# Kernel optimization log

Hardware: AMD Instinct MI355X
Metric: run time of the kernel (lower is better)

Reference implementation:

```python
import jax, jax.numpy as jnp
import numpy as np

N_VERT = 1000          # num_of_vertices; x has 3*N_VERT rows
B = 32                 # batch
IN_DIM = 64
OUT_DIMS = [64, 64, 64]


def setup_inputs() -> dict:
    key = jax.random.key(0)
    ks = jax.random.split(key, 8)
    threeN = 3 * N_VERT
    x = jax.random.normal(ks[0], (threeN, B, IN_DIM), dtype=jnp.float32)
    # dense (normalized-ish) adjacency over the localized spatio-temporal graph
    adj = jax.random.uniform(ks[1], (threeN, threeN), dtype=jnp.float32) / threeN
    inp = {"x": x, "adj": adj}
    in_d = IN_DIM
    for i, out_d in enumerate(OUT_DIMS):
        # torch Linear(in_d, 2*out_d): store as [in_d, 2*out_d] for x @ W + b
        scale = 1.0 / np.sqrt(in_d)
        inp[f"W{i}"] = jax.random.uniform(ks[2 + 2 * i], (in_d, 2 * out_d),
                                          minval=-scale, maxval=scale, dtype=jnp.float32)
        inp[f"b{i}"] = jax.random.uniform(ks[3 + 2 * i], (2 * out_d,),
                                          minval=-scale, maxval=scale, dtype=jnp.float32)
        in_d = out_d
    return inp


def _gcn_glu(adj, x, W, b, out_dim):
    # aggregate: [3N,3N] x [3N,B,C] -> [3N,B,C]
    h = jnp.einsum('nm,mbc->nbc', adj, x)
    lr = h @ W + b                       # [3N,B,2*out]
    lhs, rhs = lr[..., :out_dim], lr[..., out_dim:]
    return lhs * jax.nn.sigmoid(rhs)     # GLU


def reference(x, adj, W0, b0, W1, b1, W2, b2):
    n = x.shape[0] // 3
    Ws = [(W0, b0), (W1, b1), (W2, b2)]
    mids = []
    h = x
    for (W, b), out_d in zip(Ws, OUT_DIMS):
        h = _gcn_glu(adj, h, W, b, out_d)
        mids.append(h[n:2 * n])          # middle time-step slice [N,B,out]
    return jnp.max(jnp.stack(mids, axis=0), axis=0)  # [N,B,out]
```

## Files before the change

### kernel.cpp

```cpp
#include <hip/hip_runtime.h>
#include <stdint.h>
#include <math.h>

#define NV   3000
#define MP   3072
#define NBC  2048
#define NMID 1000

typedef unsigned short u16;
typedef short  s8vec __attribute__((ext_vector_type(8)));
typedef float  f4vec __attribute__((ext_vector_type(4)));


__device__ __forceinline__ u16 f2b(float f) {
  union { float f; unsigned int u; } v; v.f = f;
  unsigned int r = v.u + 0x7FFFu + ((v.u >> 16) & 1u);
  return (u16)(r >> 16);
}
__device__ __forceinline__ float b2f(u16 u) {
  union { unsigned int u; float f; } v; v.u = ((unsigned int)u) << 16;
  return v.f;
}

__device__ __forceinline__ void gload16(const void* g, void* l) {
  __builtin_amdgcn_global_load_lds(
      (const __attribute__((address_space(1))) void*)g,
      (__attribute__((address_space(3))) void*)l, 16, 0, 0);
}

__global__ void k_conv_adj(const float* __restrict__ adj,
                           u16* __restrict__ adjt) {
  __shared__ __align__(16) u16 tb[64][80];
  const int bx = blockIdx.x;
  const int by = blockIdx.y;
  const int t  = threadIdx.x;

  {
    const int rl = t >> 2, quad = t & 3;
    const int r  = by * 64 + rl;
    const bool rok = (r < NV);
#pragma unroll
    for (int i = 0; i < 4; ++i) {
      int c = bx * 64 + quad * 16 + i * 4;
      float4 f = {0.f, 0.f, 0.f, 0.f};
      if (rok && c < NV) f = *(const float4*)(adj + (size_t)r * NV + c);
      ushort4 o;
      o.x = f2b(f.x); o.y = f2b(f.y); o.z = f2b(f.z); o.w = f2b(f.w);
      *(ushort4*)&tb[rl][quad * 16 + i * 4] = o;
    }
  }
  __syncthreads();

  {
#pragma unroll
    for (int h = 0; h < 2; ++h) {
      int chunk = t * 2 + h;
      int sel  = chunk >> 8;
      int g    = (chunk >> 6) & 3;
      int lane = chunk & 63;
      int row  = g * 16 + (lane & 15);
      int col  = sel * 32 + (lane >> 4) * 8;
      s8vec v = *(const s8vec*)&tb[row][col];
      size_t dst = ((size_t)(by * 96 + bx * 2 + sel) * 4 + g) * 512 + lane * 8;
      *(s8vec*)(adjt + dst) = v;
    }
  }
}

__global__ void k_conv_x(const float* __restrict__ x,
                         u16* __restrict__ xt) {
  __shared__ __align__(16) u16 tb[64][72];
  int t  = threadIdx.x;
  int k0 = blockIdx.x * 64;
  int n0 = blockIdx.y * 64;
  int kl = t >> 4, ch = t & 15;
#pragma unroll
  for (int r = 0; r < 4; ++r) {
    int k = k0 + kl + r * 16;
    float4 f = {0.f, 0.f, 0.f, 0.f};
    if (k < NV) f = *(const float4*)(x + (size_t)k * NBC + n0 + ch * 4);
    tb[ch * 4 + 0][kl + r * 16] = f2b(f.x);
    tb[ch * 4 + 1][kl + r * 16] = f2b(f.y);
    tb[ch * 4 + 2][kl + r * 16] = f2b(f.z);
    tb[ch * 4 + 3][kl + r * 16] = f2b(f.w);
  }
  __syncthreads();
  int nl = t >> 4, kc = t & 15;
#pragma unroll
  for (int r = 0; r < 4; ++r) {
    int n = n0 + nl + r * 16;
    int k = k0 + kc * 4;
    ushort4 o;
    o.x = tb[nl + r * 16][kc * 4 + 0];
    o.y = tb[nl + r * 16][kc * 4 + 1];
    o.z = tb[nl + r * 16][kc * 4 + 2];
    o.w = tb[nl + r * 16][kc * 4 + 3];
    int nt = n >> 7, g = (n >> 4) & 7, lr = n & 15;
    int kk = k >> 5, hi = (k >> 3) & 3, j = k & 7;
    size_t dst = ((size_t)(nt * 96 + kk) * 8 + g) * 512 +
                 (size_t)(hi * 16 + lr) * 8 + j;
    *(ushort4*)(xt + dst) = o;
  }
}

__global__ void k_conv_w(const float* __restrict__ W0,
                         const float* __restrict__ W1,
                         const float* __restrict__ W2,
                         u16* __restrict__ Wt) {
  int e = blockIdx.x * 256 + threadIdx.x;
  const float* W = (e < 8192) ? W0 : (e < 16384) ? W1 : W2;
  int r  = e & 8191;
  int kk = r >> 12, g = (r >> 9) & 7, ln = (r >> 3) & 63, jj = r & 7;
  int c = kk * 32 + (ln >> 4) * 8 + jj;
  int j = g * 16 + (ln & 15);
  Wt[e] = f2b(W[c * 128 + j]);
}

__global__ __launch_bounds__(256) void k_gemm(
    const u16* __restrict__ At,
    const u16* __restrict__ Xt,
    u16* __restrict__ C,
    int mtbase, int chunk) {
  __shared__ __align__(16) u16 S[4 * 6144];

  const int bid = blockIdx.x;
  const int swz = (bid & 7) * chunk + (bid >> 3);
  const int mt  = mtbase + (swz >> 4);
  const int nt  = swz & 15;

  const int tid  = threadIdx.x;
  const int w    = tid >> 6;
  const int lane = tid & 63;
  const int wr   = w >> 1;
  const int wc   = w & 1;

  const u16* asrc  = At + ((size_t)mt * 96 * 4 + w) * 512 + lane * 8;
  const u16* bsrc0 = Xt + ((size_t)nt * 96 * 8 + w) * 512 + lane * 8;
  const u16* bsrc1 = Xt + ((size_t)nt * 96 * 8 + (w + 4)) * 512 + lane * 8;

  f4vec acc[2][4];
#pragma unroll
  for (int i = 0; i < 2; ++i)
#pragma unroll
    for (int j = 0; j < 4; ++j) acc[i][j] = (f4vec){0.f, 0.f, 0.f, 0.f};

  auto stage = [&](int buf, int t) {
    u16* d = S + buf * 6144;
    gload16(asrc  + (size_t)t * 2048, d + w * 512);
    gload16(bsrc0 + (size_t)t * 4096, d + 2048 + w * 512);
    gload16(bsrc1 + (size_t)t * 4096, d + 2048 + (w + 4) * 512);
  };
  auto compute = [&](int buf) {
    const u16* Ab = S + buf * 6144;
    const u16* Bb = Ab + 2048;
    s8vec a[2], b[4];
#pragma unroll
    for (int mi = 0; mi < 2; ++mi)
      a[mi] = *(const s8vec*)(Ab + (wr * 2 + mi) * 512 + lane * 8);
#pragma unroll
    for (int ni = 0; ni < 4; ++ni)
      b[ni] = *(const s8vec*)(Bb + (wc * 4 + ni) * 512 + lane * 8);
#pragma unroll
    for (int mi = 0; mi < 2; ++mi)
#pragma unroll
      for (int ni = 0; ni < 4; ++ni)
        acc[mi][ni] = __builtin_amdgcn_mfma_f32_16x16x32_bf16(
            a[mi], b[ni], acc[mi][ni], 0, 0, 0);
  };

  stage(0, 0); stage(1, 1); stage(2, 2);

#pragma unroll 1
  for (int t = 0; t < 92; t += 4) {
#pragma unroll
    for (int u = 0; u < 4; ++u) {
      asm volatile("s_waitcnt vmcnt(6)" ::: "memory");
      asm volatile("s_barrier" ::: "memory");
      stage((t + u + 3) & 3, t + u + 3);
      compute((t + u) & 3);
    }
  }
  asm volatile("s_waitcnt vmcnt(6)" ::: "memory");
  asm volatile("s_barrier" ::: "memory");
  stage(3, 95);
  compute(0);
  asm volatile("s_waitcnt vmcnt(6)" ::: "memory");
  asm volatile("s_barrier" ::: "memory");
  compute(1);
  asm volatile("s_waitcnt vmcnt(3)" ::: "memory");
  asm volatile("s_barrier" ::: "memory");
  compute(2);
  asm volatile("s_waitcnt vmcnt(0)" ::: "memory");
  asm volatile("s_barrier" ::: "memory");
  compute(3);

  const int rl = lane & 15;
  const int rh = lane >> 4;
#pragma unroll
  for (int mi = 0; mi < 2; ++mi)
#pragma unroll
    for (int ni = 0; ni < 4; ++ni) {
      int grow = mt * 64 + wr * 32 + mi * 16 + rh * 4;
      int gcol = nt * 128 + wc * 64 + ni * 16 + rl;
      u16* cp = C + (size_t)grow * NBC + gcol;
      cp[0 * NBC] = f2b(acc[mi][ni][0]);
      cp[1 * NBC] = f2b(acc[mi][ni][1]);
      cp[2 * NBC] = f2b(acc[mi][ni][2]);
      cp[3 * NBC] = f2b(acc[mi][ni][3]);
    }
}

template <int LAYER0, int WRITEX>
__global__ __launch_bounds__(256) void k_layerB(
    const u16* __restrict__ H,
    const u16* __restrict__ Wt,
    const float* __restrict__ bias,
    u16* __restrict__ xt,
    float* __restrict__ out,
    int vt0) {
  __shared__ __align__(16) u16 Hs[2][8][64][8];

  const int vt = vt0 + blockIdx.x;
  const int b  = blockIdx.y;
  const int v0 = vt * 128;
  const int t  = threadIdx.x;

#pragma unroll
  for (int q = 0; q < 4; ++q) {
    int id = q * 256 + t;
    int v  = id >> 3;
    int cc = (id & 7) * 8;
    s8vec h = *(const s8vec*)(H + (size_t)(v0 + v) * NBC + b * 64 + cc);
    int kk = cc >> 5, g = v >> 4, ln = ((cc >> 3) & 3) * 16 + (v & 15);
    *(s8vec*)&Hs[kk][g][ln][0] = h;
  }
  __syncthreads();

  const int w    = t >> 6;
  const int lane = t & 63;
  const int wvh  = w >> 1;
  const int wc   = w & 1;

  s8vec a[4][2], bf[4][2];
#pragma unroll
  for (int mi = 0; mi < 4; ++mi)
#pragma unroll
    for (int kk = 0; kk < 2; ++kk)
      a[mi][kk] = *(const s8vec*)&Hs[kk][wvh * 4 + mi][lane][0];
#pragma unroll
  for (int ni = 0; ni < 4; ++ni) {
    int g = (ni < 2) ? (wc * 2 + ni) : (4 + wc * 2 + (ni - 2));
#pragma unroll
    for (int kk = 0; kk < 2; ++kk)
      bf[ni][kk] = *(const s8vec*)(Wt + ((size_t)(kk * 8 + g) * 64 + lane) * 8);
  }

  f4vec acc[4][4];
#pragma unroll
  for (int i = 0; i < 4; ++i)
#pragma unroll
    for (int j = 0; j < 4; ++j) acc[i][j] = (f4vec){0.f, 0.f, 0.f, 0.f};
#pragma unroll
  for (int kk = 0; kk < 2; ++kk)
#pragma unroll
    for (int mi = 0; mi < 4; ++mi)
#pragma unroll
      for (int ni = 0; ni < 4; ++ni)
        acc[mi][ni] = __builtin_amdgcn_mfma_f32_16x16x32_bf16(
            a[mi][kk], bf[ni][kk], acc[mi][ni], 0, 0, 0);

  const int lr = lane & 15;
  const int rh = lane >> 4;
#pragma unroll
  for (int mi = 0; mi < 4; ++mi) {
    const int vbase = v0 + wvh * 64 + mi * 16 + rh * 4;
#pragma unroll
    for (int np = 0; np < 2; ++np) {
      const int j  = wc * 32 + np * 16 + lr;
      const float bl = bias[j];
      const float bh = bias[j + 64];
      float vals[4];
#pragma unroll
      for (int r = 0; r < 4; ++r) {
        float lo = acc[mi][np][r] + bl;
        float hi = acc[mi][np + 2][r] + bh;
        float gv = lo / (1.0f + __expf(-hi));
        vals[r] = ((vbase + r) < NV) ? gv : 0.0f;
      }
#pragma unroll
      for (int r = 0; r < 4; ++r) {
        int vg = vbase + r;
        if (vg >= NMID && vg < 2 * NMID) {
          size_t oi = (size_t)(vg - NMID) * NBC + b * 64 + j;
          if (LAYER0) out[oi] = vals[r];
          else        out[oi] = fmaxf(out[oi], vals[r]);
        }
      }
      if (WRITEX) {
        int n   = b * 64 + j;
        int nt  = n >> 7, g2 = (n >> 4) & 7, ln2 = n & 15;
        int kk2 = vbase >> 5, hi2 = (vbase >> 3) & 3, jj0 = vbase & 7;
        ushort4 o;
        o.x = f2b(vals[0]); o.y = f2b(vals[1]);
        o.z = f2b(vals[2]); o.w = f2b(vals[3]);
        size_t dst = ((size_t)(nt * 96 + kk2) * 8 + g2) * 512 +
                     (size_t)(hi2 * 16 + ln2) * 8 + jj0;
        *(ushort4*)(xt + dst) = o;
      }
    }
  }
}

extern "C" void kernel_launch(void* const* d_in, const int* in_sizes, int n_in,
                              void* d_out, int out_size, void* d_ws, size_t ws_size,
                              hipStream_t stream) {
  const float* x   = (const float*)d_in[0];
  const float* adj = (const float*)d_in[1];
  const float* W0  = (const float*)d_in[2];
  const float* b0  = (const float*)d_in[3];
  const float* W1  = (const float*)d_in[4];
  const float* b1  = (const float*)d_in[5];
  const float* W2  = (const float*)d_in[6];
  const float* b2  = (const float*)d_in[7];
  float* out = (float*)d_out;

  char* ws = (char*)d_ws;
  u16* adjt = (u16*)ws;
  u16* xa   = (u16*)(ws + 18874368);
  u16* xb   = (u16*)(ws + 18874368 + 12582912);
  u16* hb   = (u16*)(ws + 18874368 + 2 * 12582912);
  u16* Wt   = (u16*)(ws + 18874368 + 3 * 12582912);

  k_conv_adj<<<dim3(48, 48), 256, 0, stream>>>(adj, adjt);
  k_conv_x<<<dim3(48, 32), 256, 0, stream>>>(x, xa);
  k_conv_w<<<96, 256, 0, stream>>>(W0, W1, W2, Wt);

  k_gemm<<<768, 256, 0, stream>>>(adjt, xa, hb, 0, 96);
  k_layerB<1, 1><<<dim3(24, 32), 256, 0, stream>>>(hb, Wt, b0, xb, out, 0);
  k_gemm<<<768, 256, 0, stream>>>(adjt, xb, hb, 0, 96);
  k_layerB<0, 1><<<dim3(24, 32), 256, 0, stream>>>(hb, Wt + 8192, b1, xa, out, 0);
  k_gemm<<<288, 256, 0, stream>>>(adjt, xa, hb, 14, 36);
  k_layerB<0, 0><<<dim3(9, 32), 256, 0, stream>>>(hb, Wt + 16384, b2, xb, out, 7);
}
```

Before: 196.5 us.

## Enlarge GEMM tile to 192x128 with split-K and sum partials in layer kernel

```diff
diff --git a/kernel.cpp b/kernel.cpp
--- a/kernel.cpp
+++ b/kernel.cpp
@@ -116,17 +116,24 @@
   Wt[e] = f2b(W[c * 128 + j]);
 }
 
-__global__ __launch_bounds__(256) void k_gemm(
+__global__ __launch_bounds__(256, 2) void k_gemm(
     const u16* __restrict__ At,
     const u16* __restrict__ Xt,
-    u16* __restrict__ C,
-    int mtbase, int chunk) {
-  __shared__ __align__(16) u16 S[4 * 6144];
+    u16* __restrict__ C0,
+    u16* __restrict__ C1,
+    int m64base,
+    int nmt,
+    int crow0,
+    int chunk) {
+  __shared__ __align__(16) u16 S[3 * 10240];
 
   const int bid = blockIdx.x;
   const int swz = (bid & 7) * chunk + (bid >> 3);
-  const int mt  = mtbase + (swz >> 4);
   const int nt  = swz & 15;
+  const int mk  = swz >> 4;
+  const int ks  = (mk >= nmt) ? 1 : 0;
+  const int mt  = mk - ks * nmt;
+  const int kt0 = ks * 48;
 
   const int tid  = threadIdx.x;
   const int w    = tid >> 6;
@@ -134,75 +141,86 @@
   const int wr   = w >> 1;
   const int wc   = w & 1;
 
-  const u16* asrc  = At + ((size_t)mt * 96 * 4 + w) * 512 + lane * 8;
-  const u16* bsrc0 = Xt + ((size_t)nt * 96 * 8 + w) * 512 + lane * 8;
-  const u16* bsrc1 = Xt + ((size_t)nt * 96 * 8 + (w + 4)) * 512 + lane * 8;
-
-  f4vec acc[2][4];
-#pragma unroll
-  for (int i = 0; i < 2; ++i)
+  const int c0 = w * 5;
+  const u16* src[5];
+  int stp[5];
+#pragma unroll
+  for (int i = 0; i < 5; ++i) {
+    int c = c0 + i;
+    if (c < 12) {
+      int m64 = m64base + mt * 3 + (c >> 2);
+      src[i] = At + ((size_t)(m64 * 96 + kt0) * 4 + (c & 3)) * 512 + lane * 8;
+      stp[i] = 2048;
+    } else {
+      src[i] = Xt + ((size_t)(nt * 96 + kt0) * 8 + (c - 12)) * 512 + lane * 8;
+      stp[i] = 4096;
+    }
+  }
+
+  f4vec acc[6][4];
+#pragma unroll
+  for (int i = 0; i < 6; ++i)
 #pragma unroll
     for (int j = 0; j < 4; ++j) acc[i][j] = (f4vec){0.f, 0.f, 0.f, 0.f};
 
   auto stage = [&](int buf, int t) {
-    u16* d = S + buf * 6144;
-    gload16(asrc  + (size_t)t * 2048, d + w * 512);
-    gload16(bsrc0 + (size_t)t * 4096, d + 2048 + w * 512);
-    gload16(bsrc1 + (size_t)t * 4096, d + 2048 + (w + 4) * 512);
+    u16* d = S + buf * 10240 + c0 * 512;
+#pragma unroll
+    for (int i = 0; i < 5; ++i)
+      gload16(src[i] + (size_t)t * stp[i], d + i * 512);
   };
   auto compute = [&](int buf) {
-    const u16* Ab = S + buf * 6144;
-    const u16* Bb = Ab + 2048;
-    s8vec a[2], b[4];
-#pragma unroll
-    for (int mi = 0; mi < 2; ++mi)
-      a[mi] = *(const s8vec*)(Ab + (wr * 2 + mi) * 512 + lane * 8);
+    const u16* Ab = S + buf * 10240 + (wr * 6) * 512 + lane * 8;
+    const u16* Bb = S + buf * 10240 + 6144 + (wc * 4) * 512 + lane * 8;
+    s8vec a[6], b[4];
+#pragma unroll
+    for (int mi = 0; mi < 6; ++mi)
+      a[mi] = *(const s8vec*)(Ab + mi * 512);
 #pragma unroll
     for (int ni = 0; ni < 4; ++ni)
-      b[ni] = *(const s8vec*)(Bb + (wc * 4 + ni) * 512 + lane * 8);
-#pragma unroll
-    for (int mi = 0; mi < 2; ++mi)
+      b[ni] = *(const s8vec*)(Bb + ni * 512);
+#pragma unroll
+    for (int mi = 0; mi < 6; ++mi)
 #pragma unroll
       for (int ni = 0; ni < 4; ++ni)
         acc[mi][ni] = __builtin_amdgcn_mfma_f32_16x16x32_bf16(
             a[mi], b[ni], acc[mi][ni], 0, 0, 0);
   };
 
-  stage(0, 0); stage(1, 1); stage(2, 2);
+  stage(0, 0); stage(1, 1);
 
 #pragma unroll 1
-  for (int t = 0; t < 92; t += 4) {
-#pragma unroll
-    for (int u = 0; u < 4; ++u) {
-      asm volatile("s_waitcnt vmcnt(6)" ::: "memory");
+  for (int t = 0; t < 45; t += 3) {
+#pragma unroll
+    for (int u = 0; u < 3; ++u) {
+      asm volatile("s_waitcnt vmcnt(5)" ::: "memory");
       asm volatile("s_barrier" ::: "memory");
-      stage((t + u + 3) & 3, t + u + 3);
-      compute((t + u) & 3);
-    }
-  }
-  asm volatile("s_waitcnt vmcnt(6)" ::: "memory");
+      stage((u + 2) % 3, t + u + 2);
+      compute(u);
+    }
+  }
+  asm volatile("s_waitcnt vmcnt(5)" ::: "memory");
   asm volatile("s_barrier" ::: "memory");
-  stage(3, 95);
+  stage(2, 47);
   compute(0);
-  asm volatile("s_waitcnt vmcnt(6)" ::: "memory");
+  asm volatile("s_waitcnt vmcnt(5)" ::: "memory");
   asm volatile("s_barrier" ::: "memory");
   compute(1);
-  asm volatile("s_waitcnt vmcnt(3)" ::: "memory");
+  asm volatile("s_waitcnt vmcnt(0)" ::: "memory");
   asm volatile("s_barrier" ::: "memory");
   compute(2);
-  asm volatile("s_waitcnt vmcnt(0)" ::: "memory");
-  asm volatile("s_barrier" ::: "memory");
-  compute(3);
-
+
+  u16* Cs = ks ? C1 : C0;
   const int rl = lane & 15;
   const int rh = lane >> 4;
-#pragma unroll
-  for (int mi = 0; mi < 2; ++mi)
+  const int mrow0 = m64base * 64 + mt * 192 + wr * 96 - crow0;
+#pragma unroll
+  for (int mi = 0; mi < 6; ++mi)
 #pragma unroll
     for (int ni = 0; ni < 4; ++ni) {
-      int grow = mt * 64 + wr * 32 + mi * 16 + rh * 4;
+      int grow = mrow0 + mi * 16 + rh * 4;
       int gcol = nt * 128 + wc * 64 + ni * 16 + rl;
-      u16* cp = C + (size_t)grow * NBC + gcol;
+      u16* cp = Cs + (size_t)grow * NBC + gcol;
       cp[0 * NBC] = f2b(acc[mi][ni][0]);
       cp[1 * NBC] = f2b(acc[mi][ni][1]);
       cp[2 * NBC] = f2b(acc[mi][ni][2]);
@@ -212,13 +230,14 @@
 
 template <int LAYER0, int WRITEX>
 __global__ __launch_bounds__(256) void k_layerB(
-    const u16* __restrict__ H,
+    const u16* __restrict__ H0,
+    const u16* __restrict__ H1,
     const u16* __restrict__ Wt,
     const float* __restrict__ bias,
     u16* __restrict__ xt,
     float* __restrict__ out,
     int vt0) {
-  __shared__ __align__(16) u16 Hs[2][8][64][8];
+  __shared__ __align__(16) u16 Hs[2][2][8][64][8];
 
   const int vt = vt0 + blockIdx.x;
   const int b  = blockIdx.y;
@@ -226,13 +245,17 @@
   const int t  = threadIdx.x;
 
 #pragma unroll
-  for (int q = 0; q < 4; ++q) {
-    int id = q * 256 + t;
-    int v  = id >> 3;
-    int cc = (id & 7) * 8;
-    s8vec h = *(const s8vec*)(H + (size_t)(v0 + v) * NBC + b * 64 + cc);
-    int kk = cc >> 5, g = v >> 4, ln = ((cc >> 3) & 3) * 16 + (v & 15);
-    *(s8vec*)&Hs[kk][g][ln][0] = h;
+  for (int h = 0; h < 2; ++h) {
+    const u16* H = h ? H1 : H0;
+#pragma unroll
+    for (int q = 0; q < 4; ++q) {
+      int id = q * 256 + t;
+      int v  = id >> 3;
+      int cc = (id & 7) * 8;
+      s8vec hh = *(const s8vec*)(H + (size_t)(v0 + v) * NBC + b * 64 + cc);
+      int kk = cc >> 5, g = v >> 4, ln = ((cc >> 3) & 3) * 16 + (v & 15);
+      *(s8vec*)&Hs[h][kk][g][ln][0] = hh;
+    }
   }
   __syncthreads();
 
@@ -241,12 +264,7 @@
   const int wvh  = w >> 1;
   const int wc   = w & 1;
 
-  s8vec a[4][2], bf[4][2];
-#pragma unroll
-  for (int mi = 0; mi < 4; ++mi)
-#pragma unroll
-    for (int kk = 0; kk < 2; ++kk)
-      a[mi][kk] = *(const s8vec*)&Hs[kk][wvh * 4 + mi][lane][0];
+  s8vec bf[4][2];
 #pragma unroll
   for (int ni = 0; ni < 4; ++ni) {
     int g = (ni < 2) ? (wc * 2 + ni) : (4 + wc * 2 + (ni - 2));
@@ -260,14 +278,22 @@
   for (int i = 0; i < 4; ++i)
 #pragma unroll
     for (int j = 0; j < 4; ++j) acc[i][j] = (f4vec){0.f, 0.f, 0.f, 0.f};
-#pragma unroll
-  for (int kk = 0; kk < 2; ++kk)
-#pragma unroll
-    for (int mi = 0; mi < 4; ++mi)
-#pragma unroll
-      for (int ni = 0; ni < 4; ++ni)
-        acc[mi][ni] = __builtin_amdgcn_mfma_f32_16x16x32_bf16(
-            a[mi][kk], bf[ni][kk], acc[mi][ni], 0, 0, 0);
+
+#pragma unroll
+  for (int h = 0; h < 2; ++h)
+#pragma unroll
+    for (int kk = 0; kk < 2; ++kk) {
+      s8vec a[4];
+#pragma unroll
+      for (int mi = 0; mi < 4; ++mi)
+        a[mi] = *(const s8vec*)&Hs[h][kk][wvh * 4 + mi][lane][0];
+#pragma unroll
+      for (int mi = 0; mi < 4; ++mi)
+#pragma unroll
+        for (int ni = 0; ni < 4; ++ni)
+          acc[mi][ni] = __builtin_amdgcn_mfma_f32_16x16x32_bf16(
+              a[mi], bf[ni][kk], acc[mi][ni], 0, 0, 0);
+    }
 
   const int lr = lane & 15;
   const int rh = lane >> 4;
@@ -335,10 +361,11 @@
   k_conv_x<<<dim3(48, 32), 256, 0, stream>>>(x, xa);
   k_conv_w<<<96, 256, 0, stream>>>(W0, W1, W2, Wt);
 
-  k_gemm<<<768, 256, 0, stream>>>(adjt, xa, hb, 0, 96);
-  k_layerB<1, 1><<<dim3(24, 32), 256, 0, stream>>>(hb, Wt, b0, xb, out, 0);
-  k_gemm<<<768, 256, 0, stream>>>(adjt, xb, hb, 0, 96);
-  k_layerB<0, 1><<<dim3(24, 32), 256, 0, stream>>>(hb, Wt + 8192, b1, xa, out, 0);
-  k_gemm<<<288, 256, 0, stream>>>(adjt, xa, hb, 14, 36);
-  k_layerB<0, 0><<<dim3(9, 32), 256, 0, stream>>>(hb, Wt + 16384, b2, xb, out, 7);
-}
+  k_gemm<<<512, 256, 0, stream>>>(adjt, xa, hb, xb, 0, 16, 0, 64);
+  k_layerB<1, 1><<<dim3(24, 32), 256, 0, stream>>>(hb, xb, Wt, b0, xa, out, 0);
+  k_gemm<<<512, 256, 0, stream>>>(adjt, xa, hb, xb, 0, 16, 0, 64);
+  k_layerB<0, 1><<<dim3(24, 32), 256, 0, stream>>>(hb, xb, Wt + 8192, b1, xa, out, 0);
+  k_gemm<<<192, 256, 0, stream>>>(adjt, xa, hb, xb, 14, 6, 896, 24);
+  k_layerB<0, 0><<<dim3(9, 32), 256, 0, stream>>>(
+      hb - (size_t)896 * NBC, xb - (size_t)896 * NBC, Wt + 16384, b2, xa, out, 7);
+}
```

After: 175.5 us. 10.7% less time.
